# Kernel tuning notes

Hardware: AMD Instinct MI355X
Metric: run time of the kernel (lower is better)

The kernel has to match this reference:

```python
import jax, jax.numpy as jnp
import numpy as np

_INV_SQRT_2PI = 1.0 / np.sqrt(2.0 * np.pi)


def dtriple(w, noise, scale):
    # stochastic ternary: triple(w - scale*noise) = (q>1) - (q<-1)
    q = w - scale * noise
    return (q > 1).astype(jnp.float32) - (q < -1).astype(jnp.float32)


def setup_inputs() -> dict:
    key = jax.random.key(0)
    ks = jax.random.split(key, 5)
    B, D_IN, D_H, D_OUT = 4096, 1024, 16384, 3 * 32 * 32
    return {
        "x": jax.random.normal(ks[0], (B, D_IN), dtype=jnp.float32),
        "w1": jax.random.normal(ks[1], (D_IN, D_H), dtype=jnp.float32),
        "s1": jnp.ones((D_H,), dtype=jnp.float32) / 32.0,
        "b1": jnp.zeros((D_H,), dtype=jnp.float32),
        "w2": jax.random.normal(ks[2], (D_H, D_OUT), dtype=jnp.float32),
        "s2": jnp.ones((D_OUT,), dtype=jnp.float32) / np.sqrt(D_OUT).astype(np.float32),
        "b2": jnp.zeros((D_OUT,), dtype=jnp.float32),
        "n1": jax.random.normal(ks[3], (D_IN, D_H), dtype=jnp.float32),
        "n2": jax.random.normal(ks[4], (D_H, D_OUT), dtype=jnp.float32),
        "scale": 1,
    }


def reference(x, w1, s1, b1, w2, s2, b2, n1, n2, scale):
    scale = jnp.float32(scale)
    weight1 = s1 * dtriple(w1, n1, scale)          # [1024, 16384]
    h = jnp.tanh(x @ weight1 + b1)                 # [B, 16384]
    weight2 = s2 * dtriple(w2, n2, scale)          # [16384, 3072]
    out = h @ weight2 + b2                         # [B, 3072]
    return out.reshape((-1, 3, 32, 32))
```

## Files before the change

kernel.cpp:

```cpp
#include <hip/hip_runtime.h>


typedef __bf16 bf16x8 __attribute__((ext_vector_type(8)));
typedef float f32x16 __attribute__((ext_vector_type(16)));

#define AS1 __attribute__((address_space(1)))
#define AS3 __attribute__((address_space(3)))

__device__ __forceinline__ void gload_lds16(const void* g, void* l) {
    __builtin_amdgcn_global_load_lds((AS1 const void*)g, (AS3 void*)l, 16, 0, 0);
}

__device__ __forceinline__ unsigned short f2bf(float f) {
    union { float f; unsigned int u; } v; v.f = f;
    unsigned int u = v.u;
    unsigned int r = u + 0x7fffu + ((u >> 16) & 1u);
    return (unsigned short)(r >> 16);
}

__device__ __forceinline__ unsigned short tern_bf(float q) {
    return (q > 1.f) ? 0x3F80u : ((q < -1.f) ? 0xBF80u : 0u);
}

__device__ __forceinline__ float load_scale(const void* p) {
    int i = *(const int*)p;
    if (i >= -1000000 && i <= 1000000) return (float)i;
    union { int i; float f; } v; v.i = i; return v.f;
}

__device__ __forceinline__ float tanh_fast(float x) {
    float e = __expf(2.0f * x);
    return 1.0f - 2.0f * __builtin_amdgcn_rcpf(e + 1.0f);
}

__global__ __launch_bounds__(256) void pack_x_kernel(
    const float* __restrict__ x, unsigned short* __restrict__ out)
{
    const int kt = blockIdx.x, mt = blockIdx.y, tid = threadIdx.x;
    unsigned short* chunk = out + (size_t)(mt * 32 + kt) * 4096;
#pragma unroll
    for (int it = 0; it < 2; it++) {
        int g = tid + it * 256;
        int s = g >> 7, r = g & 127, h = (r >> 6) & 1, ln = r & 63;
        int m = s * 32 + (ln & 31), k = h * 16 + (ln >> 5) * 8;
        const float* src = x + (size_t)(mt * 128 + m) * 1024 + kt * 32 + k;
        float4 v0 = *(const float4*)src;
        float4 v1 = *(const float4*)(src + 4);
        unsigned int w0 = (unsigned int)f2bf(v0.x) | ((unsigned int)f2bf(v0.y) << 16);
        unsigned int w1 = (unsigned int)f2bf(v0.z) | ((unsigned int)f2bf(v0.w) << 16);
        unsigned int w2 = (unsigned int)f2bf(v1.x) | ((unsigned int)f2bf(v1.y) << 16);
        unsigned int w3 = (unsigned int)f2bf(v1.z) | ((unsigned int)f2bf(v1.w) << 16);
        uint4 o; o.x = w0; o.y = w1; o.z = w2; o.w = w3;
        *(uint4*)&chunk[(size_t)g * 8] = o;
    }
}

__global__ __launch_bounds__(256) void quant_pack_w(
    const float* __restrict__ w, const float* __restrict__ nz,
    const void* __restrict__ scale_ptr,
    unsigned short* __restrict__ out, int N, int Kt)
{
    __shared__ unsigned short lt[128 * 34];
    const int kt = blockIdx.x, nt = blockIdx.y, tid = threadIdx.x;
    const float scale = load_scale(scale_ptr);
#pragma unroll
    for (int it = 0; it < 4; it++) {
        int p = it * 1024 + tid * 4;
        int kr = p >> 7, nc = p & 127;
        size_t g = (size_t)(kt * 32 + kr) * N + nt * 128 + nc;
        float4 wv = *(const float4*)(w + g);
        float4 nv = *(const float4*)(nz + g);
        lt[(nc + 0) * 34 + kr] = tern_bf(wv.x - scale * nv.x);
        lt[(nc + 1) * 34 + kr] = tern_bf(wv.y - scale * nv.y);
        lt[(nc + 2) * 34 + kr] = tern_bf(wv.z - scale * nv.z);
        lt[(nc + 3) * 34 + kr] = tern_bf(wv.w - scale * nv.w);
    }
    __syncthreads();
    unsigned short* chunk = out + (size_t)(nt * Kt + kt) * 4096;
#pragma unroll
    for (int it = 0; it < 2; it++) {
        int g = tid + it * 256;
        int s = g >> 7, r = g & 127, h = (r >> 6) & 1, ln = r & 63;
        int n = s * 32 + (ln & 31), k = h * 16 + (ln >> 5) * 8;
        const unsigned int* p32 = (const unsigned int*)&lt[n * 34 + k];
        uint4 o; o.x = p32[0]; o.y = p32[1]; o.z = p32[2]; o.w = p32[3];
        *(uint4*)&chunk[(size_t)g * 8] = o;
    }
}


#define VMCNT(n) asm volatile("s_waitcnt vmcnt(" #n ")" ::: "memory")
#define BARRIER() { asm volatile("" ::: "memory"); __builtin_amdgcn_s_barrier(); asm volatile("" ::: "memory"); }

#define RD_FRAG(dst, HALF, SUB, P)                                            \
    dst[0] = *(const bf16x8*)&lds[P][HALF][(SUB)*1024 + lane*8];              \
    dst[1] = *(const bf16x8*)&lds[P][HALF][(SUB)*1024 + 512 + lane*8];        \
    dst[2] = *(const bf16x8*)&lds[P][HALF][4096 + (SUB)*1024 + lane*8];       \
    dst[3] = *(const bf16x8*)&lds[P][HALF][4096 + (SUB)*1024 + 512 + lane*8];

#define MFMA4(ci, cj, av, bv)                                                 \
    acc[ci][cj] = __builtin_amdgcn_mfma_f32_32x32x16_bf16(av[0], bv[0], acc[ci][cj], 0,0,0); \
    acc[ci][cj] = __builtin_amdgcn_mfma_f32_32x32x16_bf16(av[1], bv[1], acc[ci][cj], 0,0,0); \
    acc[ci][cj] = __builtin_amdgcn_mfma_f32_32x32x16_bf16(av[2], bv[2], acc[ci][cj], 0,0,0); \
    acc[ci][cj] = __builtin_amdgcn_mfma_f32_32x32x16_bf16(av[3], bv[3], acc[ci][cj], 0,0,0);

#define GSTEP(P, Q, T, W0, W1, DO_STAGE, LAST)                                \
  { RD_FRAG(fa0, 0, sA, P); RD_FRAG(fa1, 0, sA + 1, P);                       \
    RD_FRAG(fb0, 2, sB, P);                                                   \
    if (DO_STAGE) STAGE(Q, 0, (T) + 1);                                       \
    W0; BARRIER();                                                            \
    __builtin_amdgcn_s_setprio(1);                                            \
    MFMA4(0, 0, fa0, fb0); MFMA4(1, 0, fa1, fb0);                             \
    __builtin_amdgcn_s_setprio(0);                                            \
    RD_FRAG(fb1, 3, sB, P);                                                   \
    if (DO_STAGE) STAGE(Q, 2, (T) + 1);                                       \
    W1; BARRIER();                                                            \
    __builtin_amdgcn_s_setprio(1);                                            \
    MFMA4(0, 1, fa0, fb1); MFMA4(1, 1, fa1, fb1);                             \
    __builtin_amdgcn_s_setprio(0);                                            \
    RD_FRAG(fa0, 1, sA, P); RD_FRAG(fa1, 1, sA + 1, P);                       \
    if (DO_STAGE) STAGE(Q, 3, (T) + 1);                                       \
    BARRIER();                                                                \
    __builtin_amdgcn_s_setprio(1);                                            \
    MFMA4(2, 1, fa0, fb1); MFMA4(3, 1, fa1, fb1);                             \
    __builtin_amdgcn_s_setprio(0);                                            \
    if (DO_STAGE) STAGE(Q, 1, (T) + 1);                                       \
    if (!(LAST)) { VMCNT(4); }                                                \
    BARRIER();                                                                \
    __builtin_amdgcn_s_setprio(1);                                            \
    MFMA4(2, 0, fa0, fb0); MFMA4(3, 0, fa1, fb0);                             \
    __builtin_amdgcn_s_setprio(0);                                            \
  }

__global__ __launch_bounds__(512, 2) void gemm1_256_kernel(
    const unsigned short* __restrict__ Ap,
    const unsigned short* __restrict__ Bp,
    unsigned short* __restrict__ Hq,
    const float* __restrict__ s1v, const float* __restrict__ b1v)
{
    __shared__ unsigned short lds[2][4][8192];
    const int tid = threadIdx.x;
    const int lane = tid & 63, wave = tid >> 6;
    const int bid0 = blockIdx.x + 16 * blockIdx.y;
    const int wg = (bid0 & 7) * 128 + (bid0 >> 3);
    const int NT = wg & 15;
    const int MT = wg >> 4;
    const int wm = ((wave >> 2) & 1) * 64;
    const int sA = wm >> 5;
    const int sB = wave & 3;

    f32x16 acc[4][2] = {};

    const unsigned short* Ab = Ap + ((size_t)(2 * MT) * 32) * 4096;
    const unsigned short* Bb = Bp + ((size_t)(2 * NT) * 32) * 4096;

    auto STAGE = [&](int q, int half, int t) {
        const unsigned short* g = (half < 2)
            ? (Ab + ((size_t)(half * 32 + 2 * t)) * 4096)
            : (Bb + ((size_t)((half - 2) * 32 + 2 * t)) * 4096);
        unsigned short* l = &lds[q][half][0];
        gload_lds16(g + tid * 8,        l + tid * 8);
        gload_lds16(g + 4096 + tid * 8, l + 4096 + tid * 8);
    };

    bf16x8 fa0[4], fa1[4], fb0[4], fb1[4];

    STAGE(0, 0, 0); STAGE(0, 2, 0); STAGE(0, 3, 0); STAGE(0, 1, 0);
    VMCNT(4);
    BARRIER();

    for (int t = 0; t < 14; t += 2) {
        GSTEP(0, 1, t,     VMCNT(4), VMCNT(4), true, false);
        GSTEP(1, 0, t + 1, VMCNT(4), VMCNT(4), true, false);
    }
    GSTEP(0, 1, 14, VMCNT(4), VMCNT(4), true,  false);
    GSTEP(1, 0, 15, VMCNT(2), VMCNT(0), false, true);

    __syncthreads();

    const int mloc = lane & 31, hi = lane >> 5;
    unsigned int* stg32 = (unsigned int*)&lds[0][0][0];
#pragma unroll
    for (int i = 0; i < 4; i++) {
        const int kc  = (i >> 1) * 4 + sA + (i & 1);
        const int k2b = MT * 256 + (i >> 1) * 128 + wm + (i & 1) * 32;
#pragma unroll
        for (int j = 0; j < 2; j++) {
#pragma unroll
            for (int c = 0; c < 8; c++) {
                const int n1off = 8 * (c >> 1) + 4 * hi + 2 * (c & 1);
                const int n1g = k2b + n1off;
                float t0 = tanh_fast(s1v[n1g]     * acc[i][j][2 * c]     + b1v[n1g]);
                float t1 = tanh_fast(s1v[n1g + 1] * acc[i][j][2 * c + 1] + b1v[n1g + 1]);
                unsigned int pw = (unsigned int)f2bf(t0)
                                | ((unsigned int)f2bf(t1) << 16);
                const int a32 = (j * 8 + kc) * 2048 + sB * 512
                              + ((c >> 2) & 1) * 256 + ((c >> 1) & 1) * 128
                              + mloc * 4 + 2 * hi + (c & 1);
                stg32[a32] = pw;
            }
        }
    }
    __syncthreads();

#pragma unroll
    for (int mg = 0; mg < 2; mg++) {
        uint4* dst = (uint4*)(Hq + ((size_t)(2 * NT + mg) * 512 + MT * 8) * 4096);
        const uint4* src = (const uint4*)&lds[0][0][0];
#pragma unroll
        for (int it = 0; it < 8; it++)
            dst[it * 512 + tid] = src[mg * 4096 + it * 512 + tid];
    }
}

__global__ __launch_bounds__(512, 2) void gemm2_256_kernel(
    const unsigned short* __restrict__ Ap,
    const unsigned short* __restrict__ Bp,
    float* __restrict__ out,
    const float* __restrict__ s2, const float* __restrict__ b2,
    int nstep)
{
    __shared__ unsigned short lds[2][4][8192];
    const int tid = threadIdx.x;
    const int lane = tid & 63, wave = tid >> 6;
    const int bid0 = blockIdx.x + 12 * blockIdx.y;
    const int wg = (bid0 & 7) * 24 + (bid0 >> 3);
    const int NT = wg % 12;
    const int MT = wg / 12;
    const int wm = ((wave >> 2) & 1) * 64;
    const int sA = wm >> 5;
    const int sB = wave & 3;

    f32x16 acc[4][2] = {};

    const unsigned short* Ab = Ap + ((size_t)(2 * MT) * 512) * 4096;
    const unsigned short* Bb = Bp + ((size_t)(2 * NT) * 512) * 4096;

    auto STAGE = [&](int q, int half, int t) {
        const unsigned short* g = (half < 2)
            ? (Ab + ((size_t)(half * 512 + 2 * t)) * 4096)
            : (Bb + ((size_t)((half - 2) * 512 + 2 * t)) * 4096);
        unsigned short* l = &lds[q][half][0];
        gload_lds16(g + tid * 8,        l + tid * 8);
        gload_lds16(g + 4096 + tid * 8, l + 4096 + tid * 8);
    };

    bf16x8 fa0[4], fa1[4], fb0[4], fb1[4];

    STAGE(0, 0, 0); STAGE(0, 2, 0); STAGE(0, 3, 0); STAGE(0, 1, 0);
    VMCNT(4);
    BARRIER();

    for (int t = 0; t < nstep - 2; t += 2) {
        GSTEP(0, 1, t,     VMCNT(4), VMCNT(4), true, false);
        GSTEP(1, 0, t + 1, VMCNT(4), VMCNT(4), true, false);
    }
    GSTEP(0, 1, nstep - 2, VMCNT(4), VMCNT(4), true,  false);
    GSTEP(1, 0, nstep - 1, VMCNT(2), VMCNT(0), false, true);

    const int l31 = lane & 31;
    const int rowb = 4 * (lane >> 5);
#pragma unroll
    for (int j = 0; j < 2; j++) {
        int n = NT * 256 + j * 128 + sB * 32 + l31;
        float sc = s2[n], bb = b2[n];
#pragma unroll
        for (int i = 0; i < 4; i++) {
            int mbase = MT * 256 + (i >> 1) * 128 + wm + (i & 1) * 32;
#pragma unroll
            for (int reg = 0; reg < 16; reg++) {
                int m = mbase + (reg & 3) + 8 * (reg >> 2) + rowb;
                out[(size_t)m * 3072 + n] = sc * acc[i][j][reg] + bb;
            }
        }
    }
}

extern "C" void kernel_launch(void* const* d_in, const int* in_sizes, int n_in,
                              void* d_out, int out_size, void* d_ws, size_t ws_size,
                              hipStream_t stream) {
    const float* x  = (const float*)d_in[0];
    const float* w1 = (const float*)d_in[1];
    const float* s1 = (const float*)d_in[2];
    const float* b1 = (const float*)d_in[3];
    const float* w2 = (const float*)d_in[4];
    const float* s2 = (const float*)d_in[5];
    const float* b2 = (const float*)d_in[6];
    const float* n1 = (const float*)d_in[7];
    const float* n2 = (const float*)d_in[8];
    const void* scale_p = d_in[9];
    float* out = (float*)d_out;

    if (ws_size < (264ull << 20)) return;
    unsigned char* ws = (unsigned char*)d_ws;
    unsigned short* xq  = (unsigned short*)(ws);
    unsigned short* w1q = (unsigned short*)(ws + (8ull << 20));
    unsigned short* hq  = (unsigned short*)(ws + (40ull << 20));
    unsigned short* w2q = (unsigned short*)(ws + (168ull << 20));

    pack_x_kernel<<<dim3(32, 32), 256, 0, stream>>>(x, xq);
    quant_pack_w<<<dim3(32, 128), 256, 0, stream>>>(w1, n1, scale_p, w1q, 16384, 32);
    quant_pack_w<<<dim3(512, 24), 256, 0, stream>>>(w2, n2, scale_p, w2q, 3072, 512);

    gemm1_256_kernel<<<dim3(16, 64), 512, 0, stream>>>(w1q, xq, hq, s1, b1);
    gemm2_256_kernel<<<dim3(12, 16), 512, 0, stream>>>(hq, w2q, out, s2, b2, 256);
}
```

Before: 1.031 ms.

## Reorder LDS fragment reads after barriers and drop two barriers per step

The pipelined GEMM step macro in both GEMM kernels is restructured. Each step now issues the next global-to-LDS stage first, then waits and hits a barrier, and only then reads all A and B fragments of the current buffer. This cuts the barriers per step from four to two and removes the prologue wait and barrier. The vmcnt waits are re-derived so each half is complete before it is read, but with fewer barriers the cross-wave visibility and overwrite ordering between buffers becomes tighter.

```diff
diff --git a/kernel.cpp b/kernel.cpp
--- a/kernel.cpp
+++ b/kernel.cpp
@@ -104,33 +104,35 @@
     acc[ci][cj] = __builtin_amdgcn_mfma_f32_32x32x16_bf16(av[2], bv[2], acc[ci][cj], 0,0,0); \
     acc[ci][cj] = __builtin_amdgcn_mfma_f32_32x32x16_bf16(av[3], bv[3], acc[ci][cj], 0,0,0);
 
-#define GSTEP(P, Q, T, W0, W1, DO_STAGE, LAST)                                \
-  { RD_FRAG(fa0, 0, sA, P); RD_FRAG(fa1, 0, sA + 1, P);                       \
-    RD_FRAG(fb0, 2, sB, P);                                                   \
+#define GSTEP(P, Q, T, WA, WB, WC, DO_STAGE)                                  \
+  {                                                   \
     if (DO_STAGE) STAGE(Q, 0, (T) + 1);                                       \
-    W0; BARRIER();                                                            \
+    WA; BARRIER();                                                            \
+    RD_FRAG(fa0, 0, sA, P); RD_FRAG(fa1, 0, sA + 1, P);                       \
+    RD_FRAG(fb0, 2, sB, P); RD_FRAG(fb1, 3, sB, P);                           \
     __builtin_amdgcn_s_setprio(1);                                            \
     MFMA4(0, 0, fa0, fb0); MFMA4(1, 0, fa1, fb0);                             \
     __builtin_amdgcn_s_setprio(0);                                            \
-    RD_FRAG(fb1, 3, sB, P);                                                   \
     if (DO_STAGE) STAGE(Q, 2, (T) + 1);                                       \
-    W1; BARRIER();                                                            \
+    WB;                                                                       \
     __builtin_amdgcn_s_setprio(1);                                            \
     MFMA4(0, 1, fa0, fb1); MFMA4(1, 1, fa1, fb1);                             \
     __builtin_amdgcn_s_setprio(0);                                            \
-    RD_FRAG(fa0, 1, sA, P); RD_FRAG(fa1, 1, sA + 1, P);                       \
+                                                      \
     if (DO_STAGE) STAGE(Q, 3, (T) + 1);                                       \
     BARRIER();                                                                \
+    RD_FRAG(fa0, 1, sA, P); RD_FRAG(fa1, 1, sA + 1, P);                       \
     __builtin_amdgcn_s_setprio(1);                                            \
     MFMA4(2, 1, fa0, fb1); MFMA4(3, 1, fa1, fb1);                             \
     __builtin_amdgcn_s_setprio(0);                                            \
     if (DO_STAGE) STAGE(Q, 1, (T) + 1);                                       \
-    if (!(LAST)) { VMCNT(4); }                                                \
-    BARRIER();                                                                \
+    WC;                                                                       \
     __builtin_amdgcn_s_setprio(1);                                            \
     MFMA4(2, 0, fa0, fb0); MFMA4(3, 0, fa1, fb0);                             \
     __builtin_amdgcn_s_setprio(0);                                            \
   }
+
+#define NOWAIT ((void)0)
 
 __global__ __launch_bounds__(512, 2) void gemm1_256_kernel(
     const unsigned short* __restrict__ Ap,
@@ -166,15 +168,13 @@
     bf16x8 fa0[4], fa1[4], fb0[4], fb1[4];
 
     STAGE(0, 0, 0); STAGE(0, 2, 0); STAGE(0, 3, 0); STAGE(0, 1, 0);
-    VMCNT(4);
-    BARRIER();
 
     for (int t = 0; t < 14; t += 2) {
-        GSTEP(0, 1, t,     VMCNT(4), VMCNT(4), true, false);
-        GSTEP(1, 0, t + 1, VMCNT(4), VMCNT(4), true, false);
-    }
-    GSTEP(0, 1, 14, VMCNT(4), VMCNT(4), true,  false);
-    GSTEP(1, 0, 15, VMCNT(2), VMCNT(0), false, true);
+        GSTEP(0, 1, t,     VMCNT(4), VMCNT(4), VMCNT(4), true);
+        GSTEP(1, 0, t + 1, VMCNT(4), VMCNT(4), VMCNT(4), true);
+    }
+    GSTEP(0, 1, 14, VMCNT(4), VMCNT(4), VMCNT(4), true);
+    GSTEP(1, 0, 15, VMCNT(2), VMCNT(0), NOWAIT,  false);
 
     __syncthreads();
 
@@ -248,15 +248,13 @@
     bf16x8 fa0[4], fa1[4], fb0[4], fb1[4];
 
     STAGE(0, 0, 0); STAGE(0, 2, 0); STAGE(0, 3, 0); STAGE(0, 1, 0);
-    VMCNT(4);
-    BARRIER();
 
     for (int t = 0; t < nstep - 2; t += 2) {
-        GSTEP(0, 1, t,     VMCNT(4), VMCNT(4), true, false);
-        GSTEP(1, 0, t + 1, VMCNT(4), VMCNT(4), true, false);
-    }
-    GSTEP(0, 1, nstep - 2, VMCNT(4), VMCNT(4), true,  false);
-    GSTEP(1, 0, nstep - 1, VMCNT(2), VMCNT(0), false, true);
+        GSTEP(0, 1, t,     VMCNT(4), VMCNT(4), VMCNT(4), true);
+        GSTEP(1, 0, t + 1, VMCNT(4), VMCNT(4), VMCNT(4), true);
+    }
+    GSTEP(0, 1, nstep - 2, VMCNT(4), VMCNT(4), VMCNT(4), true);
+    GSTEP(1, 0, nstep - 1, VMCNT(2), VMCNT(0), NOWAIT,  false);
 
     const int l31 = lane & 31;
     const int rowb = 4 * (lane >> 5);
```

Result: no change. 1.028 ms (-0.3%).
